# Performance work log

Measured on AMD Instinct MI355X. Metric: run time of the kernel, lower is better.

Reference implementation:

```python
import jax, jax.numpy as jnp
import numpy as np

B, T, D, A = 64, 2048, 512, 128

def setup_inputs() -> dict:
    key = jax.random.key(0)
    k_x, k_w1, k_b1, k_w2, k_b2 = jax.random.split(key, 5)
    s1 = 1.0 / np.sqrt(D)
    s2 = 1.0 / np.sqrt(A)
    return {
        "x": jax.random.normal(k_x, (B, T, D), dtype=jnp.float32),
        "W1": jax.random.uniform(k_w1, (D, A), minval=-s1, maxval=s1, dtype=jnp.float32),
        "b1": jax.random.uniform(k_b1, (A,), minval=-s1, maxval=s1, dtype=jnp.float32),
        "W2": jax.random.uniform(k_w2, (A, 1), minval=-s2, maxval=s2, dtype=jnp.float32),
        "b2": jax.random.uniform(k_b2, (1,), minval=-s2, maxval=s2, dtype=jnp.float32),
    }

def reference(x, W1, b1, W2, b2):
    # attention scores: [B, T, 1]
    h = jnp.tanh(jnp.einsum('btd,da->bta', x, W1) + b1)
    scores = jnp.einsum('bta,ao->bto', h, W2) + b2
    w = jax.nn.softmax(scores, axis=1)              # [B, T, 1]
    mu = jnp.sum(x * w, axis=1)                     # [B, D]
    var = jnp.sum((x - mu[:, None, :]) ** 2 * w, axis=1)
    std = jnp.sqrt(var + 1e-6)
    return jnp.concatenate([mu, std], axis=-1)      # [B, 2D]
```

## Files before the change

### kernel.cpp

```cpp
#include <hip/hip_runtime.h>
#include <hip/hip_bf16.h>
#include <math.h>

#define B_ 64
#define T_ 2048
#define D_ 512
#define A_ 128

#define CHUNK  16
#define NCHUNK 16
#define SEG    (CHUNK*NCHUNK)
#define NBLK   (B_*(T_/SEG))

typedef __bf16 bf16x8 __attribute__((ext_vector_type(8)));
typedef float  f32x4  __attribute__((ext_vector_type(4)));

__global__ __launch_bounds__(256) void prep_kernel(
    const float* __restrict__ W1, __hip_bfloat16* __restrict__ W1T)
{
    int idx = blockIdx.x * 256 + threadIdx.x;
    int k = idx >> 7;
    int n = idx & 127;
    W1T[n * D_ + k] = __float2bfloat16(W1[idx]);
}

__device__ inline bf16x8 cvt8(float4 a, float4 b) {
    bf16x8 r;
    r[0] = (__bf16)a.x; r[1] = (__bf16)a.y; r[2] = (__bf16)a.z; r[3] = (__bf16)a.w;
    r[4] = (__bf16)b.x; r[5] = (__bf16)b.y; r[6] = (__bf16)b.z; r[7] = (__bf16)b.w;
    return r;
}

__device__ inline float fast_tanh(float v) {
    v = fminf(fmaxf(v, -15.f), 15.f);
    float e = __expf(2.f * v);
    return (e - 1.f) / (e + 1.f);
}

typedef __attribute__((address_space(1))) const void gas_t;
typedef __attribute__((address_space(3))) void las_t;
#define GLOAD_LDS16(g, l) \
    __builtin_amdgcn_global_load_lds((gas_t*)(g), (las_t*)(l), 16, 0, 0)

__global__ __launch_bounds__(256, 2) void fused_kernel(
    const float* __restrict__ x, const __hip_bfloat16* __restrict__ W1T_,
    const float* __restrict__ b1, const float* __restrict__ W2,
    const float* __restrict__ b2,
    float* __restrict__ pS, float* __restrict__ pmu, float* __restrict__ pm2)
{
    __shared__ __align__(16) float xs[2][CHUNK * D_];
    __shared__ __align__(16) float parr[4][16];

    const __bf16* W1T = (const __bf16*)W1T_;
    const int tid  = threadIdx.x;
    const int wv   = tid >> 6;
    const int lane = tid & 63;
    const int col  = lane & 15;
    const int kgrp = lane >> 4;

    const int bk  = blockIdx.x;
    const int b   = bk >> 3;
    const int seg = bk & 7;
    const float* xb = x + ((long)b * T_ + (long)seg * SEG) * D_;

    bf16x8 af[2][16];
#pragma unroll
    for (int mtl = 0; mtl < 2; mtl++) {
        const __bf16* wp = W1T + (long)((2*wv + mtl)*16 + col) * D_ + kgrp*8;
#pragma unroll
        for (int ks = 0; ks < 16; ks++)
            af[mtl][ks] = *(const bf16x8*)(wp + ks*32);
    }
    float b1v[2][4], w2v[2][4];
#pragma unroll
    for (int mtl = 0; mtl < 2; mtl++)
#pragma unroll
        for (int r = 0; r < 4; r++) {
            int n = (2*wv + mtl)*16 + kgrp*4 + r;
            b1v[mtl][r] = b1[n];
            w2v[mtl][r] = W2[n];
        }
    const float bias2 = b2[0];

    float mu0 = 0.f, mu1 = 0.f, m20 = 0.f, m21 = 0.f, su = 0.f;

    auto STAGE = [&](int bufi, int c) {
        const float* src = xb + (long)c * (CHUNK * D_);
        float* dstbase = &xs[bufi][0];
#pragma unroll
        for (int j = 0; j < 8; j++) {
            int G = j*256 + tid;
            int t = G >> 7;
            int g = G & 127;
            const float* gp = src + t*D_ + ((g ^ (t & 7)) << 2);
            float* lp = dstbase + ((j*256 + wv*64) << 2);
            GLOAD_LDS16(gp, lp);
        }
    };

    STAGE(0, 0);
    int cur = 0;

    for (int c = 0; c < NCHUNK; c++) {
        if (c + 1 < NCHUNK) {
            STAGE(cur ^ 1, c + 1);
            asm volatile("s_waitcnt vmcnt(8)" ::: "memory");
        } else {
            asm volatile("s_waitcnt vmcnt(0)" ::: "memory");
        }
        __builtin_amdgcn_s_barrier();
        asm volatile("" ::: "memory");

        const float* bufp = &xs[cur][0];

        f32x4 acc[2];
        acc[0] = (f32x4){0.f, 0.f, 0.f, 0.f};
        acc[1] = (f32x4){0.f, 0.f, 0.f, 0.f};

#pragma unroll
        for (int ks = 0; ks < 16; ks++) {
            const int m  = col & 7;
            const int gb = ks*8 + kgrp*2;
            float4 aa = *(const float4*)(bufp + (col << 9) + (((gb    ) ^ m) << 2));
            float4 bb = *(const float4*)(bufp + (col << 9) + (((gb + 1) ^ m) << 2));
            bf16x8 bfr = cvt8(aa, bb);
            acc[0] = __builtin_amdgcn_mfma_f32_16x16x32_bf16(af[0][ks], bfr, acc[0], 0, 0, 0);
            acc[1] = __builtin_amdgcn_mfma_f32_16x16x32_bf16(af[1][ks], bfr, acc[1], 0, 0, 0);
        }

        float p0 = 0.f;
#pragma unroll
        for (int mtl = 0; mtl < 2; mtl++)
#pragma unroll
            for (int r = 0; r < 4; r++)
                p0 += fast_tanh(acc[mtl][r] + b1v[mtl][r]) * w2v[mtl][r];
        p0 += __shfl_xor(p0, 16, 64);
        p0 += __shfl_xor(p0, 32, 64);
        if (lane < 16) parr[wv][lane] = p0;
        asm volatile("s_waitcnt lgkmcnt(0)" ::: "memory");
        __builtin_amdgcn_s_barrier();
        asm volatile("" ::: "memory");

        float u[16];
#pragma unroll
        for (int q = 0; q < 4; q++) {
            float4 v0 = *(const float4*)&parr[0][q*4];
            float4 v1 = *(const float4*)&parr[1][q*4];
            float4 v2 = *(const float4*)&parr[2][q*4];
            float4 v3 = *(const float4*)&parr[3][q*4];
            u[q*4+0] = __expf(v0.x + v1.x + v2.x + v3.x + bias2);
            u[q*4+1] = __expf(v0.y + v1.y + v2.y + v3.y + bias2);
            u[q*4+2] = __expf(v0.z + v1.z + v2.z + v3.z + bias2);
            u[q*4+3] = __expf(v0.w + v1.w + v2.w + v3.w + bias2);
        }
#pragma unroll
        for (int t = 0; t < 16; t++) su += u[t];

        const int gacc = tid >> 1;
        const int fo   = (tid & 1) << 1;
#pragma unroll
        for (int t = 0; t < 16; t++) {
            const float* pp = bufp + (t << 9) + ((gacc ^ (t & 7)) << 2) + fo;
            float2 xv = *(const float2*)pp;
            mu0 = fmaf(u[t], xv.x, mu0);
            mu1 = fmaf(u[t], xv.y, mu1);
            m20 = fmaf(u[t] * xv.x, xv.x, m20);
            m21 = fmaf(u[t] * xv.y, xv.y, m21);
        }
        asm volatile("" ::: "memory");
        __builtin_amdgcn_s_barrier();
        asm volatile("" ::: "memory");

        cur ^= 1;
    }

    const int d0 = tid * 2;
    pmu[(long)bk * D_ + d0]     = mu0;
    pmu[(long)bk * D_ + d0 + 1] = mu1;
    pm2[(long)bk * D_ + d0]     = m20;
    pm2[(long)bk * D_ + d0 + 1] = m21;
    if (tid == 0) pS[bk] = su;
}

__global__ __launch_bounds__(256) void merge_kernel(
    const float* __restrict__ pS, const float* __restrict__ pmu,
    const float* __restrict__ pm2, float* __restrict__ out)
{
    const int b = blockIdx.x, tid = threadIdx.x;
    float S = 0.f;
#pragma unroll
    for (int c = 0; c < 8; c++) S += pS[b*8 + c];
    const float inv = 1.f / S;

    const int d0 = tid * 2;
    float mu0 = 0.f, mu1 = 0.f, m20 = 0.f, m21 = 0.f;
#pragma unroll
    for (int c = 0; c < 8; c++) {
        const float* pb = pmu + (long)(b*8 + c) * D_ + d0;
        const float* qb = pm2 + (long)(b*8 + c) * D_ + d0;
        mu0 += pb[0]; mu1 += pb[1];
        m20 += qb[0]; m21 += qb[1];
    }
    mu0 *= inv; mu1 *= inv; m20 *= inv; m21 *= inv;

    float* ob = out + (long)b * (2 * D_);
    ob[d0]     = mu0;
    ob[d0 + 1] = mu1;
    ob[D_ + d0]     = sqrtf(fmaxf(m20 - mu0 * mu0, 0.f) + 1e-6f);
    ob[D_ + d0 + 1] = sqrtf(fmaxf(m21 - mu1 * mu1, 0.f) + 1e-6f);
}

extern "C" void kernel_launch(void* const* d_in, const int* in_sizes, int n_in,
                              void* d_out, int out_size, void* d_ws, size_t ws_size,
                              hipStream_t stream) {
    const float* x  = (const float*)d_in[0];
    const float* W1 = (const float*)d_in[1];
    const float* b1 = (const float*)d_in[2];
    const float* W2 = (const float*)d_in[3];
    const float* b2 = (const float*)d_in[4];
    float* out = (float*)d_out;

    float* ws = (float*)d_ws;
    float* pS  = ws;
    float* pmu = ws + 512;
    float* pm2 = pmu + 512L * D_;
    __hip_bfloat16* W1T = (__hip_bfloat16*)(pm2 + 512L * D_);

    prep_kernel<<<256, 256, 0, stream>>>(W1, W1T);
    fused_kernel<<<NBLK, 256, 0, stream>>>(x, W1T, b1, W2, b2, pS, pmu, pm2);
    merge_kernel<<<B_, 256, 0, stream>>>(pS, pmu, pm2, out);
}
```

Measured before the change: 392.6 us.

## Fuse weight prep and merge into main kernel via last-block atomic counter

Removes the separate W1 transpose/convert kernel: each block now loads W1 in fp32 directly with strided reads and converts it to bf16 fragments in registers. Also removes the merge kernel: after writing its partials, each block bumps a per-batch atomic counter, and the last of the 8 blocks for a batch reduces the partials and writes the output. This cuts two kernel launches and their gaps, at the cost of redundant W1 loads in every block. The counter reset done by block 0 inside the same launch relies on block scheduling order and could race.

Measured after the change: 467.2 us. +19.0%, slower.

```diff
diff --git a/kernel.cpp b/kernel.cpp
--- a/kernel.cpp
+++ b/kernel.cpp
@@ -14,15 +14,6 @@
 
 typedef __bf16 bf16x8 __attribute__((ext_vector_type(8)));
 typedef float  f32x4  __attribute__((ext_vector_type(4)));
-
-__global__ __launch_bounds__(256) void prep_kernel(
-    const float* __restrict__ W1, __hip_bfloat16* __restrict__ W1T)
-{
-    int idx = blockIdx.x * 256 + threadIdx.x;
-    int k = idx >> 7;
-    int n = idx & 127;
-    W1T[n * D_ + k] = __float2bfloat16(W1[idx]);
-}
 
 __device__ inline bf16x8 cvt8(float4 a, float4 b) {
     bf16x8 r;
@@ -43,15 +34,16 @@
     __builtin_amdgcn_global_load_lds((gas_t*)(g), (las_t*)(l), 16, 0, 0)
 
 __global__ __launch_bounds__(256, 2) void fused_kernel(
-    const float* __restrict__ x, const __hip_bfloat16* __restrict__ W1T_,
+    const float* __restrict__ x, const float* __restrict__ W1,
     const float* __restrict__ b1, const float* __restrict__ W2,
     const float* __restrict__ b2,
-    float* __restrict__ pS, float* __restrict__ pmu, float* __restrict__ pm2)
+    float* __restrict__ pS, float* __restrict__ pmu, float* __restrict__ pm2,
+    int* __restrict__ counter, float* __restrict__ out)
 {
     __shared__ __align__(16) float xs[2][CHUNK * D_];
     __shared__ __align__(16) float parr[4][16];
-
-    const __bf16* W1T = (const __bf16*)W1T_;
+    __shared__ int is_last;
+
     const int tid  = threadIdx.x;
     const int wv   = tid >> 6;
     const int lane = tid & 63;
@@ -63,13 +55,24 @@
     const int seg = bk & 7;
     const float* xb = x + ((long)b * T_ + (long)seg * SEG) * D_;
 
+    if (bk == 0) {
+        if (tid < B_) counter[tid] = 0;
+        __threadfence();
+    }
+
     bf16x8 af[2][16];
 #pragma unroll
     for (int mtl = 0; mtl < 2; mtl++) {
-        const __bf16* wp = W1T + (long)((2*wv + mtl)*16 + col) * D_ + kgrp*8;
-#pragma unroll
-        for (int ks = 0; ks < 16; ks++)
-            af[mtl][ks] = *(const bf16x8*)(wp + ks*32);
+        const int n = (2*wv + mtl)*16 + col;
+#pragma unroll
+        for (int ks = 0; ks < 16; ks++) {
+            const float* wp = W1 + (long)(kgrp*8 + ks*32) * A_ + n;
+            bf16x8 r;
+#pragma unroll
+            for (int j = 0; j < 8; j++)
+                r[j] = (__bf16)wp[j * A_];
+            af[mtl][ks] = r;
+        }
     }
     float b1v[2][4], w2v[2][4];
 #pragma unroll
@@ -180,34 +183,36 @@
     pm2[(long)bk * D_ + d0]     = m20;
     pm2[(long)bk * D_ + d0 + 1] = m21;
     if (tid == 0) pS[bk] = su;
-}
-
-__global__ __launch_bounds__(256) void merge_kernel(
-    const float* __restrict__ pS, const float* __restrict__ pmu,
-    const float* __restrict__ pm2, float* __restrict__ out)
-{
-    const int b = blockIdx.x, tid = threadIdx.x;
+
+    __threadfence();
+    if (tid == 0) {
+        int old = atomicAdd(&counter[b], 1);
+        is_last = (old == 7);
+    }
+    __syncthreads();
+    if (!is_last) return;
+    __threadfence();
+
     float S = 0.f;
 #pragma unroll
-    for (int c = 0; c < 8; c++) S += pS[b*8 + c];
+    for (int c8 = 0; c8 < 8; c8++) S += pS[b*8 + c8];
     const float inv = 1.f / S;
 
-    const int d0 = tid * 2;
-    float mu0 = 0.f, mu1 = 0.f, m20 = 0.f, m21 = 0.f;
-#pragma unroll
-    for (int c = 0; c < 8; c++) {
-        const float* pb = pmu + (long)(b*8 + c) * D_ + d0;
-        const float* qb = pm2 + (long)(b*8 + c) * D_ + d0;
-        mu0 += pb[0]; mu1 += pb[1];
-        m20 += qb[0]; m21 += qb[1];
-    }
-    mu0 *= inv; mu1 *= inv; m20 *= inv; m21 *= inv;
+    float fmu0 = 0.f, fmu1 = 0.f, fm20 = 0.f, fm21 = 0.f;
+#pragma unroll
+    for (int c8 = 0; c8 < 8; c8++) {
+        const float* pb = pmu + (long)(b*8 + c8) * D_ + d0;
+        const float* qb = pm2 + (long)(b*8 + c8) * D_ + d0;
+        fmu0 += pb[0]; fmu1 += pb[1];
+        fm20 += qb[0]; fm21 += qb[1];
+    }
+    fmu0 *= inv; fmu1 *= inv; fm20 *= inv; fm21 *= inv;
 
     float* ob = out + (long)b * (2 * D_);
-    ob[d0]     = mu0;
-    ob[d0 + 1] = mu1;
-    ob[D_ + d0]     = sqrtf(fmaxf(m20 - mu0 * mu0, 0.f) + 1e-6f);
-    ob[D_ + d0 + 1] = sqrtf(fmaxf(m21 - mu1 * mu1, 0.f) + 1e-6f);
+    ob[d0]     = fmu0;
+    ob[d0 + 1] = fmu1;
+    ob[D_ + d0]     = sqrtf(fmaxf(fm20 - fmu0 * fmu0, 0.f) + 1e-6f);
+    ob[D_ + d0 + 1] = sqrtf(fmaxf(fm21 - fmu1 * fmu1, 0.f) + 1e-6f);
 }
 
 extern "C" void kernel_launch(void* const* d_in, const int* in_sizes, int n_in,
@@ -223,10 +228,9 @@
     float* ws = (float*)d_ws;
     float* pS  = ws;
     float* pmu = ws + 512;
-    float* pm2 = pmu + 512L * D_;
-    __hip_bfloat16* W1T = (__hip_bfloat16*)(pm2 + 512L * D_);
-
-    prep_kernel<<<256, 256, 0, stream>>>(W1, W1T);
-    fused_kernel<<<NBLK, 256, 0, stream>>>(x, W1T, b1, W2, b2, pS, pmu, pm2);
-    merge_kernel<<<B_, 256, 0, stream>>>(pS, pmu, pm2, out);
-}
+    float* pm2 = pmu + (long)NBLK * D_;
+    int*   counter = (int*)(pm2 + (long)NBLK * D_);
+
+    fused_kernel<<<NBLK, 256, 0, stream>>>(x, W1, b1, W2, b2,
+                                           pS, pmu, pm2, counter, out);
+}
```

## Replace LDS double-buffered async staging with direct global loads

Applied to the files above, without the earlier changes.

Drops the shared-memory double buffer and the global_load_lds async staging of x chunks. Each wave now reads x straight from global memory, once for the MFMA operand and again as float2 rows for the weighted moment accumulation, and relies on cache for reuse. This removes most LDS traffic and frees shared memory, which could raise occupancy. In exchange it reads x from global twice per chunk and loses the explicit prefetch overlap, so latency is exposed unless the hardware hides it.

Result: slower. 454.9 us (+15.9%).

```diff
diff --git a/kernel.cpp b/kernel.cpp
--- a/kernel.cpp
+++ b/kernel.cpp
@@ -37,18 +37,12 @@
     return (e - 1.f) / (e + 1.f);
 }
 
-typedef __attribute__((address_space(1))) const void gas_t;
-typedef __attribute__((address_space(3))) void las_t;
-#define GLOAD_LDS16(g, l) \
-    __builtin_amdgcn_global_load_lds((gas_t*)(g), (las_t*)(l), 16, 0, 0)
-
 __global__ __launch_bounds__(256, 2) void fused_kernel(
     const float* __restrict__ x, const __hip_bfloat16* __restrict__ W1T_,
     const float* __restrict__ b1, const float* __restrict__ W2,
     const float* __restrict__ b2,
     float* __restrict__ pS, float* __restrict__ pmu, float* __restrict__ pm2)
 {
-    __shared__ __align__(16) float xs[2][CHUNK * D_];
     __shared__ __align__(16) float parr[4][16];
 
     const __bf16* W1T = (const __bf16*)W1T_;
@@ -61,7 +55,7 @@
     const int bk  = blockIdx.x;
     const int b   = bk >> 3;
     const int seg = bk & 7;
-    const float* xb = x + ((long)b * T_ + (long)seg * SEG) * D_;
+    const float* xseg = x + ((long)b * T_ + (long)seg * SEG) * D_;
 
     bf16x8 af[2][16];
 #pragma unroll
@@ -83,63 +77,38 @@
     const float bias2 = b2[0];
 
     float mu0 = 0.f, mu1 = 0.f, m20 = 0.f, m21 = 0.f, su = 0.f;
-
-    auto STAGE = [&](int bufi, int c) {
-        const float* src = xb + (long)c * (CHUNK * D_);
-        float* dstbase = &xs[bufi][0];
-#pragma unroll
-        for (int j = 0; j < 8; j++) {
-            int G = j*256 + tid;
-            int t = G >> 7;
-            int g = G & 127;
-            const float* gp = src + t*D_ + ((g ^ (t & 7)) << 2);
-            float* lp = dstbase + ((j*256 + wv*64) << 2);
-            GLOAD_LDS16(gp, lp);
-        }
-    };
-
-    STAGE(0, 0);
-    int cur = 0;
+    const int d0 = tid * 2;
 
     for (int c = 0; c < NCHUNK; c++) {
-        if (c + 1 < NCHUNK) {
-            STAGE(cur ^ 1, c + 1);
-            asm volatile("s_waitcnt vmcnt(8)" ::: "memory");
-        } else {
-            asm volatile("s_waitcnt vmcnt(0)" ::: "memory");
-        }
-        __builtin_amdgcn_s_barrier();
-        asm volatile("" ::: "memory");
-
-        const float* bufp = &xs[cur][0];
-
-        f32x4 acc[2];
-        acc[0] = (f32x4){0.f, 0.f, 0.f, 0.f};
-        acc[1] = (f32x4){0.f, 0.f, 0.f, 0.f};
-
+        const float* xrow = xseg + (long)(c*CHUNK + col) * D_;
+        f32x4 acc0 = (f32x4){0.f, 0.f, 0.f, 0.f};
+        f32x4 acc1 = (f32x4){0.f, 0.f, 0.f, 0.f};
 #pragma unroll
         for (int ks = 0; ks < 16; ks++) {
-            const int m  = col & 7;
-            const int gb = ks*8 + kgrp*2;
-            float4 aa = *(const float4*)(bufp + (col << 9) + (((gb    ) ^ m) << 2));
-            float4 bb = *(const float4*)(bufp + (col << 9) + (((gb + 1) ^ m) << 2));
+            float4 aa = *(const float4*)(xrow + ks*32 + kgrp*8);
+            float4 bb = *(const float4*)(xrow + ks*32 + kgrp*8 + 4);
             bf16x8 bfr = cvt8(aa, bb);
-            acc[0] = __builtin_amdgcn_mfma_f32_16x16x32_bf16(af[0][ks], bfr, acc[0], 0, 0, 0);
-            acc[1] = __builtin_amdgcn_mfma_f32_16x16x32_bf16(af[1][ks], bfr, acc[1], 0, 0, 0);
+            acc0 = __builtin_amdgcn_mfma_f32_16x16x32_bf16(af[0][ks], bfr, acc0, 0, 0, 0);
+            acc1 = __builtin_amdgcn_mfma_f32_16x16x32_bf16(af[1][ks], bfr, acc1, 0, 0, 0);
         }
+
+        float2 xv[16];
+        const float* xd = xseg + (long)(c*CHUNK) * D_ + d0;
+#pragma unroll
+        for (int t = 0; t < CHUNK; t++)
+            xv[t] = *(const float2*)(xd + (long)t * D_);
 
         float p0 = 0.f;
 #pragma unroll
-        for (int mtl = 0; mtl < 2; mtl++)
+        for (int r = 0; r < 4; r++)
+            p0 += fast_tanh(acc0[r] + b1v[0][r]) * w2v[0][r];
 #pragma unroll
-            for (int r = 0; r < 4; r++)
-                p0 += fast_tanh(acc[mtl][r] + b1v[mtl][r]) * w2v[mtl][r];
+        for (int r = 0; r < 4; r++)
+            p0 += fast_tanh(acc1[r] + b1v[1][r]) * w2v[1][r];
         p0 += __shfl_xor(p0, 16, 64);
         p0 += __shfl_xor(p0, 32, 64);
         if (lane < 16) parr[wv][lane] = p0;
-        asm volatile("s_waitcnt lgkmcnt(0)" ::: "memory");
-        __builtin_amdgcn_s_barrier();
-        asm volatile("" ::: "memory");
+        __syncthreads();
 
         float u[16];
 #pragma unroll
@@ -154,27 +123,18 @@
             u[q*4+3] = __expf(v0.w + v1.w + v2.w + v3.w + bias2);
         }
 #pragma unroll
-        for (int t = 0; t < 16; t++) su += u[t];
+        for (int t = 0; t < CHUNK; t++) su += u[t];
+        __syncthreads();
 
-        const int gacc = tid >> 1;
-        const int fo   = (tid & 1) << 1;
 #pragma unroll
-        for (int t = 0; t < 16; t++) {
-            const float* pp = bufp + (t << 9) + ((gacc ^ (t & 7)) << 2) + fo;
-            float2 xv = *(const float2*)pp;
-            mu0 = fmaf(u[t], xv.x, mu0);
-            mu1 = fmaf(u[t], xv.y, mu1);
-            m20 = fmaf(u[t] * xv.x, xv.x, m20);
-            m21 = fmaf(u[t] * xv.y, xv.y, m21);
+        for (int t = 0; t < CHUNK; t++) {
+            mu0 = fmaf(u[t], xv[t].x, mu0);
+            mu1 = fmaf(u[t], xv[t].y, mu1);
+            m20 = fmaf(u[t] * xv[t].x, xv[t].x, m20);
+            m21 = fmaf(u[t] * xv[t].y, xv[t].y, m21);
         }
-        asm volatile("" ::: "memory");
-        __builtin_amdgcn_s_barrier();
-        asm volatile("" ::: "memory");
-
-        cur ^= 1;
     }
 
-    const int d0 = tid * 2;
     pmu[(long)bk * D_ + d0]     = mu0;
     pmu[(long)bk * D_ + d0 + 1] = mu1;
     pm2[(long)bk * D_ + d0]     = m20;
@@ -223,8 +183,8 @@
     float* ws = (float*)d_ws;
     float* pS  = ws;
     float* pmu = ws + 512;
-    float* pm2 = pmu + 512L * D_;
-    __hip_bfloat16* W1T = (__hip_bfloat16*)(pm2 + 512L * D_);
+    float* pm2 = pmu + (long)NBLK * D_;
+    __hip_bfloat16* W1T = (__hip_bfloat16*)(pm2 + (long)NBLK * D_);
 
     prep_kernel<<<256, 256, 0, stream>>>(W1, W1T);
     fused_kernel<<<NBLK, 256, 0, stream>>>(x, W1T, b1, W2, b2, pS, pmu, pm2);
```
